# Performance work log

Hardware: AMD Instinct MI355X
Metric: run time of the kernel (lower is better)

The kernel has to match this reference:

```python
import jax, jax.numpy as jnp
import numpy as np

NEG_INF = -1e9  # masked_fill value in torch code
HELP_THRESH = -1e8  # help_scores > -1e8 marks valid dependency entries


def setup_inputs() -> dict:
    key = jax.random.key(0)
    ks = jax.random.split(key, 16)
    B, S, D, H, DK = 8, 512, 1024, 16, 64
    sc = 0.02
    x = jax.random.normal(ks[0], (B, S, D), jnp.float32)
    Wq = jax.random.normal(ks[1], (D, H * DK), jnp.float32) * sc
    bq = jax.random.normal(ks[2], (H * DK,), jnp.float32) * sc
    Wk = jax.random.normal(ks[3], (D, H * DK), jnp.float32) * sc
    bk = jax.random.normal(ks[4], (H * DK,), jnp.float32) * sc
    Wv = jax.random.normal(ks[5], (D, H * DK), jnp.float32) * sc
    bv = jax.random.normal(ks[6], (H * DK,), jnp.float32) * sc
    Wo = jax.random.normal(ks[7], (H * DK, D), jnp.float32) * sc
    bo = jax.random.normal(ks[8], (D,), jnp.float32) * sc
    ln_g = jnp.ones((D,), jnp.float32)
    ln_b = jnp.zeros((D,), jnp.float32)
    help_vals = jax.random.normal(ks[9], (B, H, S, S), jnp.float32)
    help_mask = jax.random.randint(ks[10], (B, H, S, S), 0, 2).astype(jnp.int32)
    attn_mask = jax.random.randint(ks[11], (B, S, S), 0, 2).astype(bool)
    return {"x": x, "Wq": Wq, "bq": bq, "Wk": Wk, "bk": bk, "Wv": Wv,
            "bv": bv, "Wo": Wo, "bo": bo, "ln_g": ln_g, "ln_b": ln_b,
            "help_vals": help_vals, "help_mask": help_mask, "attn_mask": attn_mask}


def reference(x, Wq, bq, Wk, bk, Wv, bv, Wo, bo, ln_g, ln_b,
              help_vals, help_mask, attn_mask):
    B, S, D = x.shape
    H, DK = 16, 64
    # projections -> [B,H,S,dk]
    q = (x @ Wq + bq).reshape(B, S, H, DK).transpose(0, 2, 1, 3)
    k = (x @ Wk + bk).reshape(B, S, H, DK).transpose(0, 2, 1, 3)
    v = (x @ Wv + bv).reshape(B, S, H, DK).transpose(0, 2, 1, 3)
    scores = jnp.einsum('bhqd,bhkd->bhqk', q, k) / np.sqrt(DK).astype(np.float32)
    scores = jnp.where(attn_mask[:, None, :, :], NEG_INF, scores)
    # dependency-tree score blending (ScaledDotProductAttention)
    help_scores = jnp.where(help_mask.astype(bool), help_vals, NEG_INF)
    m = (help_scores > HELP_THRESH).astype(scores.dtype)
    dep_w = m * 0.5
    seq_w = m * 0.5 + (1.0 - m)
    scores = help_scores * dep_w + scores * seq_w
    attn = jax.nn.softmax(scores, axis=-1)
    ctx = jnp.einsum('bhqk,bhkd->bhqd', attn, v)  # [B,H,S,dv]
    ctx = ctx.transpose(0, 2, 1, 3).reshape(B, S, H * DK)
    out = ctx @ Wo + bo
    # residual + LayerNorm (input_dim == output_dim path)
    y = out + x
    mu = y.mean(-1, keepdims=True)
    var = ((y - mu) ** 2).mean(-1, keepdims=True)
    y = (y - mu) / jnp.sqrt(var + 1e-5) * ln_g + ln_b
    return y, attn
```

## Files before the change

kernel.cpp:

```cpp
#include <hip/hip_runtime.h>
#include <hip/hip_bf16.h>

typedef __bf16 bf16_t;
typedef __bf16 bf16x4 __attribute__((ext_vector_type(4)));
typedef __bf16 bf16x8 __attribute__((ext_vector_type(8)));
typedef float f32x4 __attribute__((ext_vector_type(4)));
typedef int i32x4 __attribute__((ext_vector_type(4)));


__device__ __forceinline__ f32x4 mfma16(bf16x8 a, bf16x8 b, f32x4 c) {
    return __builtin_amdgcn_mfma_f32_16x16x32_bf16(a, b, c, 0, 0, 0);
}

__device__ __forceinline__ float blendf(float s, int am, int hm, float hv) {
    s = am ? -1e9f : s;
    return hm ? 0.5f * hv + 0.5f * s : s;
}

#define GLOAD_LDS16(g, l)                                                   \
    __builtin_amdgcn_global_load_lds(                                       \
        (const __attribute__((address_space(1))) void*)(g),                 \
        (__attribute__((address_space(3))) void*)(l), 16, 0, 0)

__global__ __launch_bounds__(256) void cast_kernel(const float* __restrict__ x,
                                                   bf16_t* __restrict__ xb) {
    size_t i = ((size_t)blockIdx.x * 256 + threadIdx.x) * 4;
    float4 v = *(const float4*)(x + i);
    bf16x4 o;
    o[0] = (bf16_t)v.x; o[1] = (bf16_t)v.y; o[2] = (bf16_t)v.z; o[3] = (bf16_t)v.w;
    *(bf16x4*)(xb + i) = o;
}

__global__ __launch_bounds__(256) void transpose_kernel(const float* __restrict__ Wq,
                                                        const float* __restrict__ Wk,
                                                        const float* __restrict__ Wv,
                                                        const float* __restrict__ Wo,
                                                        bf16_t* __restrict__ Wt_base) {
    __shared__ float tile[32][33];
    const int z = blockIdx.z;
    const float* W = (z == 0) ? Wq : (z == 1) ? Wk : (z == 2) ? Wv : Wo;
    bf16_t* Wt = Wt_base + ((size_t)z << 20);
    int tx = threadIdx.x & 31, ty = threadIdx.x >> 5;
    int bx = blockIdx.x * 32, by = blockIdx.y * 32;
#pragma unroll
    for (int j = 0; j < 4; j++)
        tile[ty + j * 8][tx] = W[(size_t)(by + ty + j * 8) * 1024 + bx + tx];
    __syncthreads();
#pragma unroll
    for (int j = 0; j < 4; j++)
        Wt[(size_t)(bx + ty + j * 8) * 1024 + by + tx] = (bf16_t)tile[tx][ty + j * 8];
}

__global__ __launch_bounds__(256, 4) void gemm_qkv(const bf16_t* __restrict__ A,
                                                   const bf16_t* __restrict__ WtB,
                                                   const float* __restrict__ bq,
                                                   const float* __restrict__ bk,
                                                   const float* __restrict__ bv,
                                                   bf16_t* __restrict__ qb,
                                                   bf16_t* __restrict__ kb,
                                                   bf16_t* __restrict__ vt) {
    constexpr int K = 1024;
    __shared__ bf16_t As[2][128][32];
    __shared__ bf16_t Bs[2][128][32];
    const int z = blockIdx.z;
    const bf16_t* Bt = WtB + ((size_t)z << 20);
    const float* bias = (z == 0) ? bq : (z == 1) ? bk : bv;
    const int t = threadIdx.x;
    const int lane = t & 63, wv = t >> 6;
    const int lm = lane & 15, q4 = lane >> 4;
    const int mblk = blockIdx.y * 128, nblk = blockIdx.x * 128;
    const int mrow = (wv & 1) * 64, ncol = (wv >> 1) * 64;
    const int sr = t >> 2, sc = (t & 3) * 8;

    f32x4 acc[4][4];
#pragma unroll
    for (int r = 0; r < 4; r++)
#pragma unroll
        for (int c = 0; c < 4; c++) acc[r][c] = (f32x4){0.f, 0.f, 0.f, 0.f};

    const bf16_t* ga = &A[(size_t)(mblk + sr) * K + sc];
    const bf16_t* gb = &Bt[(size_t)(nblk + sr) * K + sc];
    GLOAD_LDS16(ga, &As[0][sr][sc]);
    GLOAD_LDS16(ga + (size_t)64 * K, &As[0][sr + 64][sc]);
    GLOAD_LDS16(gb, &Bs[0][sr][sc]);
    GLOAD_LDS16(gb + (size_t)64 * K, &Bs[0][sr + 64][sc]);
    __syncthreads();

    int cur = 0;
    for (int k0 = 0; k0 < K; k0 += 32) {
        if (k0 + 32 < K) {
            const bf16_t* ga2 = ga + k0 + 32;
            const bf16_t* gb2 = gb + k0 + 32;
            GLOAD_LDS16(ga2, &As[cur ^ 1][sr][sc]);
            GLOAD_LDS16(ga2 + (size_t)64 * K, &As[cur ^ 1][sr + 64][sc]);
            GLOAD_LDS16(gb2, &Bs[cur ^ 1][sr][sc]);
            GLOAD_LDS16(gb2 + (size_t)64 * K, &Bs[cur ^ 1][sr + 64][sc]);
        }
        bf16x8 af[4], bfr[4];
#pragma unroll
        for (int r = 0; r < 4; r++) af[r] = *(const bf16x8*)&As[cur][mrow + r * 16 + lm][q4 * 8];
#pragma unroll
        for (int c = 0; c < 4; c++) bfr[c] = *(const bf16x8*)&Bs[cur][ncol + c * 16 + lm][q4 * 8];
#pragma unroll
        for (int r = 0; r < 4; r++)
#pragma unroll
            for (int c = 0; c < 4; c++) acc[r][c] = mfma16(af[r], bfr[c], acc[r][c]);
        __syncthreads();
        cur ^= 1;
    }

#pragma unroll
    for (int r = 0; r < 4; r++)
#pragma unroll
        for (int c = 0; c < 4; c++)
#pragma unroll
            for (int i = 0; i < 4; i++) {
                int m = mblk + mrow + r * 16 + q4 * 4 + i;
                int n = nblk + ncol + c * 16 + lm;
                float v = acc[r][c][i] + bias[n];
                int b = m >> 9, s = m & 511, h = n >> 6, d = n & 63;
                if (z < 2) {
                    bf16_t* o = z ? kb : qb;
                    o[(((size_t)(b * 16 + h) * 512) + s) * 64 + d] = (bf16_t)v;
                } else {
                    vt[(((size_t)(b * 16 + h) * 64) + d) * 512 + s] = (bf16_t)v;
                }
            }
}

__global__ __launch_bounds__(256, 4) void gemm_out(const bf16_t* __restrict__ A,
                                                   const bf16_t* __restrict__ Bt,
                                                   const float* __restrict__ bias,
                                                   const float* __restrict__ resid,
                                                   float* __restrict__ outp) {
    constexpr int K = 1024, N = 1024;
    __shared__ bf16_t As[2][128][32];
    __shared__ bf16_t Bs[2][128][32];
    const int t = threadIdx.x;
    const int lane = t & 63, wv = t >> 6;
    const int lm = lane & 15, q4 = lane >> 4;
    const int mblk = blockIdx.y * 128, nblk = blockIdx.x * 128;
    const int mrow = (wv & 1) * 64, ncol = (wv >> 1) * 64;
    const int sr = t >> 2, sc = (t & 3) * 8;

    f32x4 acc[4][4];
#pragma unroll
    for (int r = 0; r < 4; r++)
#pragma unroll
        for (int c = 0; c < 4; c++) acc[r][c] = (f32x4){0.f, 0.f, 0.f, 0.f};

    const bf16_t* ga = &A[(size_t)(mblk + sr) * K + sc];
    const bf16_t* gb = &Bt[(size_t)(nblk + sr) * K + sc];
    GLOAD_LDS16(ga, &As[0][sr][sc]);
    GLOAD_LDS16(ga + (size_t)64 * K, &As[0][sr + 64][sc]);
    GLOAD_LDS16(gb, &Bs[0][sr][sc]);
    GLOAD_LDS16(gb + (size_t)64 * K, &Bs[0][sr + 64][sc]);
    __syncthreads();

    int cur = 0;
    for (int k0 = 0; k0 < K; k0 += 32) {
        if (k0 + 32 < K) {
            const bf16_t* ga2 = ga + k0 + 32;
            const bf16_t* gb2 = gb + k0 + 32;
            GLOAD_LDS16(ga2, &As[cur ^ 1][sr][sc]);
            GLOAD_LDS16(ga2 + (size_t)64 * K, &As[cur ^ 1][sr + 64][sc]);
            GLOAD_LDS16(gb2, &Bs[cur ^ 1][sr][sc]);
            GLOAD_LDS16(gb2 + (size_t)64 * K, &Bs[cur ^ 1][sr + 64][sc]);
        }
        bf16x8 af[4], bfr[4];
#pragma unroll
        for (int r = 0; r < 4; r++) af[r] = *(const bf16x8*)&As[cur][mrow + r * 16 + lm][q4 * 8];
#pragma unroll
        for (int c = 0; c < 4; c++) bfr[c] = *(const bf16x8*)&Bs[cur][ncol + c * 16 + lm][q4 * 8];
#pragma unroll
        for (int r = 0; r < 4; r++)
#pragma unroll
            for (int c = 0; c < 4; c++) acc[r][c] = mfma16(af[r], bfr[c], acc[r][c]);
        __syncthreads();
        cur ^= 1;
    }

#pragma unroll
    for (int r = 0; r < 4; r++)
#pragma unroll
        for (int c = 0; c < 4; c++)
#pragma unroll
            for (int i = 0; i < 4; i++) {
                int m = mblk + mrow + r * 16 + q4 * 4 + i;
                int n = nblk + ncol + c * 16 + lm;
                float v = acc[r][c][i] + bias[n];
                outp[(size_t)m * N + n] = v + resid[(size_t)m * N + n];
            }
}

__global__ __launch_bounds__(256, 4) void attn_fused_kernel(const bf16_t* __restrict__ Qb,
                                                            const bf16_t* __restrict__ Kb,
                                                            const bf16_t* __restrict__ Vt,
                                                            const float* __restrict__ help_vals,
                                                            const int* __restrict__ help_mask,
                                                            const int* __restrict__ attn_mask,
                                                            float* __restrict__ attn_out,
                                                            bf16_t* __restrict__ xo) {
    constexpr int SS = 516;
    const int t = threadIdx.x;
    const int lane = t & 63, wv = t >> 6;
    const int lm = lane & 15, q4 = lane >> 4;
    const int bh = blockIdx.y;
    const int b = bh >> 4, h = bh & 15;
    const int q0 = blockIdx.x * 16;
    const bf16_t* Qp = Qb + (size_t)bh * 512 * 64;
    const bf16_t* Kp = Kb + (size_t)bh * 512 * 64;
    const bf16_t* Vp = Vt + (size_t)bh * 64 * 512;

    __shared__ float S[16][SS];

    const int c0 = lane * 4, c1 = 256 + lane * 4;
    const int rbase = wv * 4;
    const size_t qrow0 = ((size_t)bh * 512 + q0 + rbase) * 512;
    const size_t arow0 = ((size_t)b * 512 + q0 + rbase) * 512;

    f32x4 hv[2][2];
    i32x4 hm[2][2], am[2][2];
    hv[0][0] = __builtin_nontemporal_load((const f32x4*)&help_vals[qrow0 + c0]);
    hv[0][1] = __builtin_nontemporal_load((const f32x4*)&help_vals[qrow0 + c1]);
    hm[0][0] = __builtin_nontemporal_load((const i32x4*)&help_mask[qrow0 + c0]);
    hm[0][1] = __builtin_nontemporal_load((const i32x4*)&help_mask[qrow0 + c1]);
    am[0][0] = *(const i32x4*)&attn_mask[arow0 + c0];
    am[0][1] = *(const i32x4*)&attn_mask[arow0 + c1];

    const bf16x8 bq0 = *(const bf16x8*)&Qp[(size_t)(q0 + lm) * 64 + q4 * 8];
    const bf16x8 bq1 = *(const bf16x8*)&Qp[(size_t)(q0 + lm) * 64 + 32 + q4 * 8];
    f32x4 acc[8];
#pragma unroll
    for (int kt = 0; kt < 8; kt++) acc[kt] = (f32x4){0.f, 0.f, 0.f, 0.f};
    __builtin_amdgcn_s_setprio(1);
#pragma unroll
    for (int kt = 0; kt < 8; kt++) {
        const int krow = wv * 128 + kt * 16 + lm;
        bf16x8 ak0 = *(const bf16x8*)&Kp[(size_t)krow * 64 + q4 * 8];
        bf16x8 ak1 = *(const bf16x8*)&Kp[(size_t)krow * 64 + 32 + q4 * 8];
        acc[kt] = mfma16(ak0, bq0, acc[kt]);
        acc[kt] = mfma16(ak1, bq1, acc[kt]);
    }
    __builtin_amdgcn_s_setprio(0);
#pragma unroll
    for (int kt = 0; kt < 8; kt++)
        *(f32x4*)&S[lm][wv * 128 + kt * 16 + q4 * 4] = acc[kt] * 0.125f;
    __syncthreads();

#pragma unroll
    for (int rr = 0; rr < 4; rr++) {
        const int sl = rr & 1, sn = sl ^ 1;
        if (rr < 3) {
            const size_t qr = qrow0 + (size_t)(rr + 1) * 512;
            const size_t ar = arow0 + (size_t)(rr + 1) * 512;
            hv[sn][0] = __builtin_nontemporal_load((const f32x4*)&help_vals[qr + c0]);
            hv[sn][1] = __builtin_nontemporal_load((const f32x4*)&help_vals[qr + c1]);
            hm[sn][0] = __builtin_nontemporal_load((const i32x4*)&help_mask[qr + c0]);
            hm[sn][1] = __builtin_nontemporal_load((const i32x4*)&help_mask[qr + c1]);
            am[sn][0] = *(const i32x4*)&attn_mask[ar + c0];
            am[sn][1] = *(const i32x4*)&attn_mask[ar + c1];
        }
        const int r = rbase + rr;
        const size_t qrow = qrow0 + (size_t)rr * 512;
        f32x4 s0 = *(const f32x4*)&S[r][c0];
        f32x4 s1 = *(const f32x4*)&S[r][c1];
        float sv[8];
#pragma unroll
        for (int i = 0; i < 4; i++) sv[i] = blendf(s0[i], am[sl][0][i], hm[sl][0][i], hv[sl][0][i]);
#pragma unroll
        for (int i = 0; i < 4; i++)
            sv[4 + i] = blendf(s1[i], am[sl][1][i], hm[sl][1][i], hv[sl][1][i]);
        float mloc = fmaxf(fmaxf(fmaxf(sv[0], sv[1]), fmaxf(sv[2], sv[3])),
                           fmaxf(fmaxf(sv[4], sv[5]), fmaxf(sv[6], sv[7])));
#pragma unroll
        for (int off = 1; off < 64; off <<= 1) mloc = fmaxf(mloc, __shfl_xor(mloc, off));
        float lsum = 0.f;
#pragma unroll
        for (int i = 0; i < 8; i++) {
            sv[i] = __expf(sv[i] - mloc);
            lsum += sv[i];
        }
#pragma unroll
        for (int off = 1; off < 64; off <<= 1) lsum += __shfl_xor(lsum, off);
        const float rinv = 1.0f / lsum;
        f32x4 o0, o1;
        o0[0] = sv[0] * rinv; o0[1] = sv[1] * rinv; o0[2] = sv[2] * rinv; o0[3] = sv[3] * rinv;
        o1[0] = sv[4] * rinv; o1[1] = sv[5] * rinv; o1[2] = sv[6] * rinv; o1[3] = sv[7] * rinv;
        *(f32x4*)&S[r][c0] = o0;
        *(f32x4*)&S[r][c1] = o1;
        __builtin_nontemporal_store(o0, (f32x4*)&attn_out[qrow + c0]);
        __builtin_nontemporal_store(o1, (f32x4*)&attn_out[qrow + c1]);
    }
    __syncthreads();

    f32x4 acc2[4];
#pragma unroll
    for (int mt = 0; mt < 4; mt++) acc2[mt] = (f32x4){0.f, 0.f, 0.f, 0.f};
    const int kb0 = wv * 128;
    __builtin_amdgcn_s_setprio(1);
#pragma unroll
    for (int C = 0; C < 4; C++) {
        f32x4 pa = *(const f32x4*)&S[lm][kb0 + C * 32 + q4 * 8];
        f32x4 pb = *(const f32x4*)&S[lm][kb0 + C * 32 + q4 * 8 + 4];
        bf16x8 pf;
        pf[0] = (bf16_t)pa[0]; pf[1] = (bf16_t)pa[1]; pf[2] = (bf16_t)pa[2]; pf[3] = (bf16_t)pa[3];
        pf[4] = (bf16_t)pb[0]; pf[5] = (bf16_t)pb[1]; pf[6] = (bf16_t)pb[2]; pf[7] = (bf16_t)pb[3];
#pragma unroll
        for (int mt = 0; mt < 4; mt++) {
            const bf16x8 vf =
                *(const bf16x8*)&Vp[(size_t)(mt * 16 + lm) * 512 + kb0 + C * 32 + q4 * 8];
            acc2[mt] = mfma16(vf, pf, acc2[mt]);
        }
    }
    __builtin_amdgcn_s_setprio(0);
    __syncthreads();

    float* redp = &S[0][0];
#pragma unroll
    for (int mt = 0; mt < 4; mt++)
        *(f32x4*)(redp + ((wv * 16 + lm) * 68 + mt * 16 + q4 * 4)) = acc2[mt];
    __syncthreads();
    {
        const int qq = t >> 4;
        const int d4 = (t & 15) * 4;
        f32x4 r0 = *(const f32x4*)(redp + ((0 * 16 + qq) * 68 + d4));
        f32x4 r1 = *(const f32x4*)(redp + ((1 * 16 + qq) * 68 + d4));
        f32x4 r2 = *(const f32x4*)(redp + ((2 * 16 + qq) * 68 + d4));
        f32x4 r3 = *(const f32x4*)(redp + ((3 * 16 + qq) * 68 + d4));
        f32x4 sum = r0 + r1 + r2 + r3;
        bf16x4 o;
        o[0] = (bf16_t)sum[0]; o[1] = (bf16_t)sum[1];
        o[2] = (bf16_t)sum[2]; o[3] = (bf16_t)sum[3];
        *(bf16x4*)&xo[((size_t)(b * 512 + q0 + qq)) * 1024 + h * 64 + d4] = o;
    }
}

__global__ __launch_bounds__(256) void layernorm_kernel(const float* __restrict__ ypre,
                                                        const float* __restrict__ g,
                                                        const float* __restrict__ bvec,
                                                        float* __restrict__ out) {
    int row = blockIdx.x;
    int t = threadIdx.x;
    float4 v = ((const float4*)(ypre + (size_t)row * 1024))[t];
    float s = v.x + v.y + v.z + v.w;
    float sq = v.x * v.x + v.y * v.y + v.z * v.z + v.w * v.w;
#pragma unroll
    for (int off = 32; off; off >>= 1) {
        s += __shfl_down(s, off);
        sq += __shfl_down(sq, off);
    }
    __shared__ float ss[4], ssq[4];
    if ((t & 63) == 0) { ss[t >> 6] = s; ssq[t >> 6] = sq; }
    __syncthreads();
    float tot = ss[0] + ss[1] + ss[2] + ss[3];
    float totq = ssq[0] + ssq[1] + ssq[2] + ssq[3];
    float mu = tot * (1.0f / 1024.0f);
    float var = totq * (1.0f / 1024.0f) - mu * mu;
    float rstd = rsqrtf(var + 1e-5f);
    float4 gg = ((const float4*)g)[t];
    float4 bb = ((const float4*)bvec)[t];
    float4 o;
    o.x = (v.x - mu) * rstd * gg.x + bb.x;
    o.y = (v.y - mu) * rstd * gg.y + bb.y;
    o.z = (v.z - mu) * rstd * gg.z + bb.z;
    o.w = (v.w - mu) * rstd * gg.w + bb.w;
    ((float4*)(out + (size_t)row * 1024))[t] = o;
}

extern "C" void kernel_launch(void* const* d_in, const int* in_sizes, int n_in,
                              void* d_out, int out_size, void* d_ws, size_t ws_size,
                              hipStream_t stream) {
    const float* x         = (const float*)d_in[0];
    const float* Wq        = (const float*)d_in[1];
    const float* bq        = (const float*)d_in[2];
    const float* Wk        = (const float*)d_in[3];
    const float* bk        = (const float*)d_in[4];
    const float* Wv        = (const float*)d_in[5];
    const float* bv        = (const float*)d_in[6];
    const float* Wo        = (const float*)d_in[7];
    const float* bo        = (const float*)d_in[8];
    const float* ln_g      = (const float*)d_in[9];
    const float* ln_b      = (const float*)d_in[10];
    const float* help_vals = (const float*)d_in[11];
    const int*   help_mask = (const int*)d_in[12];
    const int*   attn_mask = (const int*)d_in[13];

    char* ws = (char*)d_ws;
    bf16_t* xb   = (bf16_t*)(ws);
    bf16_t* wqt  = (bf16_t*)(ws + ((size_t)8 << 20));
    bf16_t* wot  = (bf16_t*)(ws + ((size_t)14 << 20));
    bf16_t* qb   = (bf16_t*)(ws + ((size_t)16 << 20));
    bf16_t* kb   = (bf16_t*)(ws + ((size_t)24 << 20));
    bf16_t* vt   = (bf16_t*)(ws + ((size_t)32 << 20));
    bf16_t* xo   = (bf16_t*)(ws + ((size_t)40 << 20));
    float*  ypre = (float*)(ws + ((size_t)48 << 20));

    float* y_out = (float*)d_out;
    float* attn_out = y_out + (size_t)4096 * 1024;

    cast_kernel<<<4096, 256, 0, stream>>>(x, xb);
    transpose_kernel<<<dim3(32, 32, 4), 256, 0, stream>>>(Wq, Wk, Wv, Wo, wqt);

    gemm_qkv<<<dim3(8, 32, 3), 256, 0, stream>>>(xb, wqt, bq, bk, bv, qb, kb, vt);

    attn_fused_kernel<<<dim3(32, 128), 256, 0, stream>>>(qb, kb, vt, help_vals, help_mask,
                                                         attn_mask, attn_out, xo);

    gemm_out<<<dim3(8, 32), 256, 0, stream>>>(xo, wot, bo, x, ypre);
    layernorm_kernel<<<4096, 256, 0, stream>>>(ypre, ln_g, ln_b, y_out);
}
```

Measured before the change: 478.2 us.

## Use 512-thread attention blocks with LDS atomic context reduction

Doubles the attention block from 4 to 8 waves, so each wave handles 64 keys and 2 softmax rows instead of 128 keys and 4 rows. The register double-buffered prefetch of help/mask rows is dropped in favour of plain per-row loads. The cross-wave PV reduction now uses LDS float atomicAdd into a zeroed ctx buffer instead of a staging pass plus a 4-way sum. This aims for more memory-level parallelism per CU in a bandwidth-bound kernel, at the cost of losing the explicit prefetch overlap and adding LDS atomic contention. The launch bounds of (512, 8) may also constrain registers.

```diff
diff --git a/kernel.cpp b/kernel.cpp
--- a/kernel.cpp
+++ b/kernel.cpp
@@ -193,7 +193,7 @@
             }
 }
 
-__global__ __launch_bounds__(256, 4) void attn_fused_kernel(const bf16_t* __restrict__ Qb,
+__global__ __launch_bounds__(512, 8) void attn_fused_kernel(const bf16_t* __restrict__ Qb,
                                                             const bf16_t* __restrict__ Kb,
                                                             const bf16_t* __restrict__ Vt,
                                                             const float* __restrict__ help_vals,
@@ -213,30 +213,19 @@
     const bf16_t* Vp = Vt + (size_t)bh * 64 * 512;
 
     __shared__ float S[16][SS];
-
-    const int c0 = lane * 4, c1 = 256 + lane * 4;
-    const int rbase = wv * 4;
-    const size_t qrow0 = ((size_t)bh * 512 + q0 + rbase) * 512;
-    const size_t arow0 = ((size_t)b * 512 + q0 + rbase) * 512;
-
-    f32x4 hv[2][2];
-    i32x4 hm[2][2], am[2][2];
-    hv[0][0] = __builtin_nontemporal_load((const f32x4*)&help_vals[qrow0 + c0]);
-    hv[0][1] = __builtin_nontemporal_load((const f32x4*)&help_vals[qrow0 + c1]);
-    hm[0][0] = __builtin_nontemporal_load((const i32x4*)&help_mask[qrow0 + c0]);
-    hm[0][1] = __builtin_nontemporal_load((const i32x4*)&help_mask[qrow0 + c1]);
-    am[0][0] = *(const i32x4*)&attn_mask[arow0 + c0];
-    am[0][1] = *(const i32x4*)&attn_mask[arow0 + c1];
+    __shared__ float ctx[16][68];
+
+    for (int i = t; i < 16 * 68; i += 512) ((float*)ctx)[i] = 0.f;
 
     const bf16x8 bq0 = *(const bf16x8*)&Qp[(size_t)(q0 + lm) * 64 + q4 * 8];
     const bf16x8 bq1 = *(const bf16x8*)&Qp[(size_t)(q0 + lm) * 64 + 32 + q4 * 8];
-    f32x4 acc[8];
-#pragma unroll
-    for (int kt = 0; kt < 8; kt++) acc[kt] = (f32x4){0.f, 0.f, 0.f, 0.f};
+    f32x4 acc[4];
+#pragma unroll
+    for (int kt = 0; kt < 4; kt++) acc[kt] = (f32x4){0.f, 0.f, 0.f, 0.f};
     __builtin_amdgcn_s_setprio(1);
 #pragma unroll
-    for (int kt = 0; kt < 8; kt++) {
-        const int krow = wv * 128 + kt * 16 + lm;
+    for (int kt = 0; kt < 4; kt++) {
+        const int krow = wv * 64 + kt * 16 + lm;
         bf16x8 ak0 = *(const bf16x8*)&Kp[(size_t)krow * 64 + q4 * 8];
         bf16x8 ak1 = *(const bf16x8*)&Kp[(size_t)krow * 64 + 32 + q4 * 8];
         acc[kt] = mfma16(ak0, bq0, acc[kt]);
@@ -244,33 +233,30 @@
     }
     __builtin_amdgcn_s_setprio(0);
 #pragma unroll
-    for (int kt = 0; kt < 8; kt++)
-        *(f32x4*)&S[lm][wv * 128 + kt * 16 + q4 * 4] = acc[kt] * 0.125f;
-    __syncthreads();
-
-#pragma unroll
-    for (int rr = 0; rr < 4; rr++) {
-        const int sl = rr & 1, sn = sl ^ 1;
-        if (rr < 3) {
-            const size_t qr = qrow0 + (size_t)(rr + 1) * 512;
-            const size_t ar = arow0 + (size_t)(rr + 1) * 512;
-            hv[sn][0] = __builtin_nontemporal_load((const f32x4*)&help_vals[qr + c0]);
-            hv[sn][1] = __builtin_nontemporal_load((const f32x4*)&help_vals[qr + c1]);
-            hm[sn][0] = __builtin_nontemporal_load((const i32x4*)&help_mask[qr + c0]);
-            hm[sn][1] = __builtin_nontemporal_load((const i32x4*)&help_mask[qr + c1]);
-            am[sn][0] = *(const i32x4*)&attn_mask[ar + c0];
-            am[sn][1] = *(const i32x4*)&attn_mask[ar + c1];
-        }
-        const int r = rbase + rr;
-        const size_t qrow = qrow0 + (size_t)rr * 512;
+    for (int kt = 0; kt < 4; kt++)
+        *(f32x4*)&S[lm][wv * 64 + kt * 16 + q4 * 4] = acc[kt] * 0.125f;
+    __syncthreads();
+
+    const int c0 = lane * 4, c1 = 256 + lane * 4;
+#pragma unroll 1
+    for (int rr = 0; rr < 2; rr++) {
+        const int r = wv * 2 + rr;
+        const int q = q0 + r;
+        const size_t qrow = ((size_t)bh * 512 + q) * 512;
+        const size_t arow = ((size_t)b * 512 + q) * 512;
+        const f32x4 hv0 = __builtin_nontemporal_load((const f32x4*)&help_vals[qrow + c0]);
+        const f32x4 hv1 = __builtin_nontemporal_load((const f32x4*)&help_vals[qrow + c1]);
+        const i32x4 hm0 = __builtin_nontemporal_load((const i32x4*)&help_mask[qrow + c0]);
+        const i32x4 hm1 = __builtin_nontemporal_load((const i32x4*)&help_mask[qrow + c1]);
+        const i32x4 am0 = *(const i32x4*)&attn_mask[arow + c0];
+        const i32x4 am1 = *(const i32x4*)&attn_mask[arow + c1];
         f32x4 s0 = *(const f32x4*)&S[r][c0];
         f32x4 s1 = *(const f32x4*)&S[r][c1];
         float sv[8];
 #pragma unroll
-        for (int i = 0; i < 4; i++) sv[i] = blendf(s0[i], am[sl][0][i], hm[sl][0][i], hv[sl][0][i]);
-#pragma unroll
-        for (int i = 0; i < 4; i++)
-            sv[4 + i] = blendf(s1[i], am[sl][1][i], hm[sl][1][i], hv[sl][1][i]);
+        for (int i = 0; i < 4; i++) sv[i] = blendf(s0[i], am0[i], hm0[i], hv0[i]);
+#pragma unroll
+        for (int i = 0; i < 4; i++) sv[4 + i] = blendf(s1[i], am1[i], hm1[i], hv1[i]);
         float mloc = fmaxf(fmaxf(fmaxf(sv[0], sv[1]), fmaxf(sv[2], sv[3])),
                            fmaxf(fmaxf(sv[4], sv[5]), fmaxf(sv[6], sv[7])));
 #pragma unroll
@@ -297,10 +283,10 @@
     f32x4 acc2[4];
 #pragma unroll
     for (int mt = 0; mt < 4; mt++) acc2[mt] = (f32x4){0.f, 0.f, 0.f, 0.f};
-    const int kb0 = wv * 128;
+    const int kb0 = wv * 64;
     __builtin_amdgcn_s_setprio(1);
 #pragma unroll
-    for (int C = 0; C < 4; C++) {
+    for (int C = 0; C < 2; C++) {
         f32x4 pa = *(const f32x4*)&S[lm][kb0 + C * 32 + q4 * 8];
         f32x4 pb = *(const f32x4*)&S[lm][kb0 + C * 32 + q4 * 8 + 4];
         bf16x8 pf;
@@ -314,21 +300,16 @@
         }
     }
     __builtin_amdgcn_s_setprio(0);
-    __syncthreads();
-
-    float* redp = &S[0][0];
 #pragma unroll
     for (int mt = 0; mt < 4; mt++)
-        *(f32x4*)(redp + ((wv * 16 + lm) * 68 + mt * 16 + q4 * 4)) = acc2[mt];
-    __syncthreads();
-    {
+#pragma unroll
+        for (int i = 0; i < 4; i++) atomicAdd(&ctx[lm][mt * 16 + q4 * 4 + i], acc2[mt][i]);
+    __syncthreads();
+
+    if (t < 256) {
         const int qq = t >> 4;
         const int d4 = (t & 15) * 4;
-        f32x4 r0 = *(const f32x4*)(redp + ((0 * 16 + qq) * 68 + d4));
-        f32x4 r1 = *(const f32x4*)(redp + ((1 * 16 + qq) * 68 + d4));
-        f32x4 r2 = *(const f32x4*)(redp + ((2 * 16 + qq) * 68 + d4));
-        f32x4 r3 = *(const f32x4*)(redp + ((3 * 16 + qq) * 68 + d4));
-        f32x4 sum = r0 + r1 + r2 + r3;
+        f32x4 sum = *(const f32x4*)&ctx[qq][d4];
         bf16x4 o;
         o[0] = (bf16_t)sum[0]; o[1] = (bf16_t)sum[1];
         o[2] = (bf16_t)sum[2]; o[3] = (bf16_t)sum[3];
@@ -404,7 +385,7 @@
 
     gemm_qkv<<<dim3(8, 32, 3), 256, 0, stream>>>(xb, wqt, bq, bk, bv, qb, kb, vt);
 
-    attn_fused_kernel<<<dim3(32, 128), 256, 0, stream>>>(qb, kb, vt, help_vals, help_mask,
+    attn_fused_kernel<<<dim3(32, 128), 512, 0, stream>>>(qb, kb, vt, help_vals, help_mask,
                                                          attn_mask, attn_out, xo);
 
     gemm_out<<<dim3(8, 32), 256, 0, stream>>>(xo, wot, bo, x, ypre);
```

Result: slower. 584.8 us (+22.3%).
